# Performance work log

Measured on AMD Instinct MI355X. Metric: run time of the kernel, lower is better.

The kernel has to match this reference:

```python
import jax, jax.numpy as jnp
import numpy as np

N = 100_000      # nodes
E = 3_200_000    # edges
B = 1024         # graphs in batch
IN = 4           # in_channels
G = 16           # GCNNodes
D = 32           # NDenseNodes


def _linear_params(k, out_f, in_f):
    s = 1.0 / np.sqrt(in_f)
    kw, kb = jax.random.split(k)
    W = jax.random.uniform(kw, (out_f, in_f), jnp.float32, -s, s)
    b = jax.random.uniform(kb, (out_f,), jnp.float32, -s, s)
    return W, b


def setup_inputs() -> dict:
    key = jax.random.key(0)
    ks = jax.random.split(key, 12)
    X = jax.random.normal(ks[0], (N, IN), jnp.float32)
    Edge_index = jax.random.randint(ks[1], (2, E), 0, N, jnp.int64)
    Edge_weight = jax.random.uniform(ks[2], (E,), jnp.float32)
    Batching = jnp.sort(jax.random.randint(ks[3], (N,), 0, B, jnp.int64))
    W1, b1 = _linear_params(ks[4], G, IN)   # Conv1 lin (PyG GCNConv: Linear no bias + bias param)
    W2, b2 = _linear_params(ks[5], G, G)    # Conv2
    C1w, C1b = _linear_params(ks[6], D, 2 * G)
    C2w, C2b = _linear_params(ks[7], D, D)
    C3w, C3b = _linear_params(ks[8], 1, D)
    R1w, R1b = _linear_params(ks[9], D, 2 * G)
    R2w, R2b = _linear_params(ks[10], D, D)
    R3w, R3b = _linear_params(ks[11], 1, D)
    return {"X": X, "Edge_index": Edge_index, "Edge_weight": Edge_weight,
            "Batching": Batching, "num_graphs": B,
            "W1": W1, "b1": b1, "W2": W2, "b2": b2,
            "C1w": C1w, "C1b": C1b, "C2w": C2w, "C2b": C2b, "C3w": C3w, "C3b": C3b,
            "R1w": R1w, "R1b": R1b, "R2w": R2w, "R2b": R2b, "R3w": R3w, "R3b": R3b}


def _gcn_conv(x, row, col, w, W, b):
    """PyG GCNConv: add self loops (weight 1), symmetric norm, x@W.T, scatter-add at col, +b."""
    n = x.shape[0]
    loop = jnp.arange(n)
    row2 = jnp.concatenate([row, loop])
    col2 = jnp.concatenate([col, loop])
    w2 = jnp.concatenate([w, jnp.ones((n,), x.dtype)])
    deg = jax.ops.segment_sum(w2, col2, num_segments=n)          # deg >= 1 via self loops
    dinv = jnp.where(deg > 0, jax.lax.rsqrt(deg), 0.0)
    norm = dinv[row2] * w2 * dinv[col2]                           # [E+n]
    xw = x @ W.T                                                  # [n, out]
    out = jax.ops.segment_sum(norm[:, None] * xw[row2], col2, num_segments=n)
    return out + b


def reference(X, Edge_index, Edge_weight, Batching, num_graphs,
              W1, b1, W2, b2, C1w, C1b, C2w, C2b, C3w, C3b,
              R1w, R1b, R2w, R2b, R3w, R3b):
    act = jax.nn.leaky_relu  # default slope 0.01, matches nn.LeakyReLU()
    row, col = Edge_index[0], Edge_index[1]
    # add_self_loops then keep only col > row  ==  zero out weights where col <= row
    w = jnp.where(col > row, Edge_weight, 0.0)

    out = act(_gcn_conv(X, row, col, w, W1, b1))
    out = act(_gcn_conv(out, row, col, w, W2, b2))

    ones = jnp.ones((out.shape[0],), out.dtype)
    cnt = jax.ops.segment_sum(ones, Batching, num_segments=num_graphs)
    outMean = jax.ops.segment_sum(out, Batching, num_segments=num_graphs) / jnp.maximum(cnt, 1.0)[:, None]
    outMax = jax.ops.segment_max(out, Batching, num_segments=num_graphs)
    pooled = jnp.concatenate([outMean, outMax], axis=1)           # [B, 2G]

    Chi0 = act(pooled @ C1w.T + C1b)
    Chi0 = act(Chi0 @ C2w.T + C2b)
    Chi0 = Chi0 @ C3w.T + C3b
    Rp = act(pooled @ R1w.T + R1b)
    Rp = act(Rp @ R2w.T + R2b)
    Rp = Rp @ R3w.T + R3b
    return jnp.concatenate([Chi0, Rp], axis=1)                    # [B, 2]
```

## Files before the change

### kernel.cpp

```cpp
#include <hip/hip_runtime.h>
#include <hip/hip_bf16.h>
#include <float.h>

#define LRELU(x) ((x) > 0.0f ? (x) : 0.01f * (x))

typedef unsigned long long u64;

__global__ __launch_bounds__(256) void k_init(const float* __restrict__ X,
                                              const float* __restrict__ W1,
                                              u64* __restrict__ deg64,
                                              float* __restrict__ xw, int N) {
    int i = blockIdx.x * blockDim.x + threadIdx.x;
    if (i >= N) return;
    deg64[i] = (u64)1 << 32;
    const float4 x = *reinterpret_cast<const float4*>(X + 4 * i);
    float o[16];
#pragma unroll
    for (int g = 0; g < 16; ++g) {
        const float4 wr = *reinterpret_cast<const float4*>(W1 + 4 * g);
        o[g] = x.x * wr.x + x.y * wr.y + x.z * wr.z + x.w * wr.w;
    }
    float4* dst = reinterpret_cast<float4*>(xw + 16 * i);
#pragma unroll
    for (int k = 0; k < 4; ++k)
        dst[k] = make_float4(o[4 * k], o[4 * k + 1], o[4 * k + 2], o[4 * k + 3]);
}

__global__ __launch_bounds__(256) void k_count(const int* __restrict__ row,
                                               const int* __restrict__ col,
                                               const float* __restrict__ w,
                                               u64* __restrict__ deg64,
                                               unsigned char* __restrict__ rank, int E) {
    int e = blockIdx.x * blockDim.x + threadIdx.x;
    if (e >= E) return;
    int r = row[e], c = col[e];
    if (c <= r) return;
    u64 add = ((u64)1 << 40) | (u64)(w[e] * 4294967296.0f);
    u64 old = atomicAdd(deg64 + c, add);
    rank[e] = (unsigned char)(old >> 40);
}

__global__ __launch_bounds__(256) void k_scan1(const u64* __restrict__ deg64,
                                               int* __restrict__ offs,
                                               int* __restrict__ partials, int N) {
    __shared__ int sm[256];
    int tid = threadIdx.x;
    int base = blockIdx.x * 1024 + tid * 4;
    int v[4];
    int s = 0;
#pragma unroll
    for (int k = 0; k < 4; ++k) {
        int idx = base + k;
        v[k] = (idx < N) ? (int)(deg64[idx] >> 40) : 0;
        s += v[k];
    }
    sm[tid] = s;
    __syncthreads();
    for (int off = 1; off < 256; off <<= 1) {
        int t = (tid >= off) ? sm[tid - off] : 0;
        __syncthreads();
        sm[tid] += t;
        __syncthreads();
    }
    int run = sm[tid] - s;
#pragma unroll
    for (int k = 0; k < 4; ++k) {
        int idx = base + k;
        if (idx < N) offs[idx] = run;
        run += v[k];
    }
    if (tid == 255) partials[blockIdx.x] = sm[255];
}

__global__ __launch_bounds__(256) void k_scan2(int* __restrict__ partials,
                                               int* __restrict__ offs, int nb, int N) {
    __shared__ int sm[256];
    int tid = threadIdx.x;
    int v = (tid < nb) ? partials[tid] : 0;
    sm[tid] = v;
    __syncthreads();
    for (int off = 1; off < 256; off <<= 1) {
        int t = (tid >= off) ? sm[tid - off] : 0;
        __syncthreads();
        sm[tid] += t;
        __syncthreads();
    }
    if (tid < nb) partials[tid] = sm[tid] - v;
    if (tid == nb - 1) offs[N] = sm[tid];
}

__global__ __launch_bounds__(256) void k_self3(int* __restrict__ offs,
                                               const int* __restrict__ partials,
                                               const u64* __restrict__ deg64,
                                               float* __restrict__ dinv,
                                               const float* __restrict__ xw,
                                               float* __restrict__ acc, int N) {
    int i = blockIdx.x * blockDim.x + threadIdx.x;
    if (i >= N) return;
    offs[i] += partials[i >> 10];
    float wsum = (float)((double)(deg64[i] & (((u64)1 << 40) - 1)) * (1.0 / 4294967296.0));
    float d = rsqrtf(wsum);
    dinv[i] = d;
    float s = d * d;
    const float4* xs = reinterpret_cast<const float4*>(xw + 16 * i);
    float4* as = reinterpret_cast<float4*>(acc + 16 * i);
#pragma unroll
    for (int k = 0; k < 4; ++k) {
        float4 v = xs[k];
        as[k] = make_float4(s * v.x, s * v.y, s * v.z, s * v.w);
    }
}

__global__ __launch_bounds__(256) void k_fill(const int* __restrict__ row,
                                              const int* __restrict__ col,
                                              const float* __restrict__ w,
                                              const float* __restrict__ dinv,
                                              const int* __restrict__ offs,
                                              const unsigned char* __restrict__ rank,
                                              int2* __restrict__ pack, int E) {
    int e = blockIdx.x * blockDim.x + threadIdx.x;
    if (e >= E) return;
    int r = row[e], c = col[e];
    if (c <= r) return;
    float nrm = dinv[r] * w[e] * dinv[c];
    int pos = offs[c] + (int)rank[e];
    pack[pos] = make_int2(r, __float_as_int(nrm));
}

__global__ __launch_bounds__(256) void k_gather(const int* __restrict__ offs,
                                                const int2* __restrict__ pack,
                                                const float* __restrict__ xw,
                                                float* __restrict__ acc, int N) {
    int t = blockIdx.x * blockDim.x + threadIdx.x;
    if (t >= 16 * N) return;
    int c = t >> 4, g = t & 15;
    int beg = offs[c], end = offs[c + 1];
    float a = acc[t];
    for (int j = beg; j < end; ++j) {
        int2 p = pack[j];
        a += __int_as_float(p.y) * xw[((size_t)p.x << 4) + g];
    }
    acc[t] = a;
}

__global__ __launch_bounds__(256) void k_mid(const float* __restrict__ b1,
                                             const float* __restrict__ W2,
                                             const float* __restrict__ dinv,
                                             float* __restrict__ xw,
                                             float* __restrict__ acc, int N) {
    int i = blockIdx.x * blockDim.x + threadIdx.x;
    if (i >= N) return;
    float h[16];
#pragma unroll
    for (int g = 0; g < 16; ++g) {
        float v = acc[16 * i + g] + b1[g];
        h[g] = LRELU(v);
    }
    float d = dinv[i];
    float s = d * d;
#pragma unroll
    for (int g = 0; g < 16; ++g) {
        float a = 0.0f;
#pragma unroll
        for (int k = 0; k < 16; ++k) a += h[k] * W2[16 * g + k];
        xw[16 * i + g] = a;
        acc[16 * i + g] = s * a;
    }
}

__global__ __launch_bounds__(256) void k_initf(const float* __restrict__ X,
                                               const float* __restrict__ W1,
                                               float* __restrict__ deg,
                                               float* __restrict__ xw, int N) {
    int i = blockIdx.x * blockDim.x + threadIdx.x;
    if (i >= N) return;
    deg[i] = 1.0f;
    const float4 x = *reinterpret_cast<const float4*>(X + 4 * i);
    float o[16];
#pragma unroll
    for (int g = 0; g < 16; ++g) {
        const float4 wr = *reinterpret_cast<const float4*>(W1 + 4 * g);
        o[g] = x.x * wr.x + x.y * wr.y + x.z * wr.z + x.w * wr.w;
    }
    float4* dst = reinterpret_cast<float4*>(xw + 16 * i);
#pragma unroll
    for (int k = 0; k < 4; ++k)
        dst[k] = make_float4(o[4 * k], o[4 * k + 1], o[4 * k + 2], o[4 * k + 3]);
}

__global__ __launch_bounds__(256) void k_degf(const int* __restrict__ row,
                                              const int* __restrict__ col,
                                              const float* __restrict__ w,
                                              float* __restrict__ deg, int E) {
    int e = blockIdx.x * blockDim.x + threadIdx.x;
    if (e >= E) return;
    int r = row[e], c = col[e];
    if (c > r) atomicAdd(deg + c, w[e]);
}

__global__ __launch_bounds__(256) void k_self(float* __restrict__ deg_dinv,
                                              const float* __restrict__ xw,
                                              float* __restrict__ acc, int N) {
    int i = blockIdx.x * blockDim.x + threadIdx.x;
    if (i >= N) return;
    float d = rsqrtf(deg_dinv[i]);
    deg_dinv[i] = d;
    float s = d * d;
    const float4* xs = reinterpret_cast<const float4*>(xw + 16 * i);
    float4* as = reinterpret_cast<float4*>(acc + 16 * i);
#pragma unroll
    for (int k = 0; k < 4; ++k) {
        float4 v = xs[k];
        as[k] = make_float4(s * v.x, s * v.y, s * v.z, s * v.w);
    }
}

__global__ __launch_bounds__(256) void k_scatter(const int* __restrict__ row,
                                                 const int* __restrict__ col,
                                                 const float* __restrict__ w,
                                                 const float* __restrict__ dinv,
                                                 const float* __restrict__ xw,
                                                 float* __restrict__ acc, int E) {
    int e = blockIdx.x * blockDim.x + threadIdx.x;
    if (e >= E) return;
    int r = row[e], c = col[e];
    if (c <= r) return;
    float nrm = dinv[r] * w[e] * dinv[c];
    const float4* xr = reinterpret_cast<const float4*>(xw + 16 * r);
    float* ac = acc + 16 * c;
#pragma unroll
    for (int k = 0; k < 4; ++k) {
        float4 v = xr[k];
        atomicAdd(ac + 4 * k + 0, nrm * v.x);
        atomicAdd(ac + 4 * k + 1, nrm * v.y);
        atomicAdd(ac + 4 * k + 2, nrm * v.z);
        atomicAdd(ac + 4 * k + 3, nrm * v.w);
    }
}

__global__ __launch_bounds__(64) void k_pool(const float* __restrict__ acc,
                                             const float* __restrict__ b2,
                                             const int* __restrict__ batching,
                                             int N,
                                             const float* __restrict__ C1w, const float* __restrict__ C1b,
                                             const float* __restrict__ C2w, const float* __restrict__ C2b,
                                             const float* __restrict__ C3w, const float* __restrict__ C3b,
                                             const float* __restrict__ R1w, const float* __restrict__ R1b,
                                             const float* __restrict__ R2w, const float* __restrict__ R2b,
                                             const float* __restrict__ R3w, const float* __restrict__ R3b,
                                             float* __restrict__ out) {
    int b = blockIdx.x;
    int t = threadIdx.x;
    __shared__ int s_se[2];
    __shared__ float sp[32];
    __shared__ float h1s[64];
    __shared__ float h2s[64];
    if (t < 2) {
        int target = b + t;
        int lo = 0, hi = N;
        while (lo < hi) {
            int mid = (lo + hi) >> 1;
            if (batching[mid] < target) lo = mid + 1; else hi = mid;
        }
        s_se[t] = lo;
    }
    __syncthreads();
    int start = s_se[0], end = s_se[1];
    int g = t & 15, sub = t >> 4;
    float bg = b2[g];
    float sum = 0.0f, mx = -FLT_MAX;
    for (int n = start + sub; n < end; n += 4) {
        float v = acc[16 * n + g] + bg;
        v = LRELU(v);
        sum += v;
        mx = fmaxf(mx, v);
    }
    sum += __shfl_down(sum, 32);
    mx = fmaxf(mx, __shfl_down(mx, 32));
    sum += __shfl_down(sum, 16);
    mx = fmaxf(mx, __shfl_down(mx, 16));
    if (t < 16) {
        float cnt = (float)(end - start);
        sp[t] = sum / fmaxf(cnt, 1.0f);
        sp[16 + t] = mx;
    }
    __syncthreads();
    int d = t & 31;
    const float* W1h = (t < 32) ? C1w : R1w;
    const float* b1h = (t < 32) ? C1b : R1b;
    float a1 = b1h[d];
#pragma unroll 4
    for (int k = 0; k < 32; ++k) a1 += sp[k] * W1h[32 * d + k];
    h1s[t] = LRELU(a1);
    __syncthreads();
    const float* W2h = (t < 32) ? C2w : R2w;
    const float* b2h = (t < 32) ? C2b : R2b;
    const float* h1base = h1s + (t < 32 ? 0 : 32);
    float a2 = b2h[d];
#pragma unroll 4
    for (int k = 0; k < 32; ++k) a2 += h1base[k] * W2h[32 * d + k];
    h2s[t] = LRELU(a2);
    __syncthreads();
    if (t == 0 || t == 32) {
        const float* w3 = (t == 0) ? C3w : R3w;
        float a3 = (t == 0) ? C3b[0] : R3b[0];
        const float* hb = h2s + t;
#pragma unroll 4
        for (int k = 0; k < 32; ++k) a3 += hb[k] * w3[k];
        out[2 * b + (t >> 5)] = a3;
    }
}

extern "C" void kernel_launch(void* const* d_in, const int* in_sizes, int n_in,
                              void* d_out, int out_size, void* d_ws, size_t ws_size,
                              hipStream_t stream) {
    const float* X   = (const float*)d_in[0];
    const int*   EI  = (const int*)d_in[1];
    const float* EW  = (const float*)d_in[2];
    const int*   Bat = (const int*)d_in[3];
    const float* W1  = (const float*)d_in[5];
    const float* b1  = (const float*)d_in[6];
    const float* W2  = (const float*)d_in[7];
    const float* b2  = (const float*)d_in[8];
    const float* C1w = (const float*)d_in[9];
    const float* C1b = (const float*)d_in[10];
    const float* C2w = (const float*)d_in[11];
    const float* C2b = (const float*)d_in[12];
    const float* C3w = (const float*)d_in[13];
    const float* C3b = (const float*)d_in[14];
    const float* R1w = (const float*)d_in[15];
    const float* R1b = (const float*)d_in[16];
    const float* R2w = (const float*)d_in[17];
    const float* R2b = (const float*)d_in[18];
    const float* R3w = (const float*)d_in[19];
    const float* R3b = (const float*)d_in[20];

    const int N = in_sizes[0] / 4;
    const int E = in_sizes[1] / 2;
    const int B = out_size / 2;
    const int* row = EI;
    const int* col = EI + E;

    float* outp = (float*)d_out;

    size_t off = 0;
    u64*   deg64 = (u64*)d_ws;            off += 2 * (size_t)N;
    float* xw    = (float*)d_ws + off;    off += 16 * (size_t)N;
    float* acc   = (float*)d_ws + off;    off += 16 * (size_t)N;
    float* dinv  = (float*)d_ws + off;    off += (size_t)N;
    int*   offs  = (int*)d_ws + off;      off += (size_t)N + 1;
    int*   part  = (int*)d_ws + off;      off += 256;
    unsigned char* rank = (unsigned char*)((int*)d_ws + off);
    off += ((size_t)E + 3) / 4;
    off = (off + 1) & ~(size_t)1;
    int2*  pack  = (int2*)((int*)d_ws + off);
    size_t needed = off * 4 + (size_t)E * 8;

    const int nb = (N + 1023) / 1024;

    dim3 blk(256);
    dim3 gN((N + 255) / 256);
    dim3 gE((E + 255) / 256);
    dim3 gNG((16 * N + 255) / 256);

    if (needed <= ws_size && nb <= 256) {
        k_init <<<gN, blk, 0, stream>>>(X, W1, deg64, xw, N);
        k_count<<<gE, blk, 0, stream>>>(row, col, EW, deg64, rank, E);
        k_scan1<<<dim3(nb), blk, 0, stream>>>(deg64, offs, part, N);
        k_scan2<<<dim3(1), blk, 0, stream>>>(part, offs, nb, N);
        k_self3<<<gN, blk, 0, stream>>>(offs, part, deg64, dinv, xw, acc, N);
        k_fill <<<gE, blk, 0, stream>>>(row, col, EW, dinv, offs, rank, pack, E);
        k_gather<<<gNG, blk, 0, stream>>>(offs, pack, xw, acc, N);
        k_mid  <<<gN, blk, 0, stream>>>(b1, W2, dinv, xw, acc, N);
        k_gather<<<gNG, blk, 0, stream>>>(offs, pack, xw, acc, N);
        k_pool<<<dim3(B), dim3(64), 0, stream>>>(acc, b2, Bat, N,
                                                 C1w, C1b, C2w, C2b, C3w, C3b,
                                                 R1w, R1b, R2w, R2b, R3w, R3b,
                                                 outp);
    } else {
        float* deg = (float*)d_ws;
        k_initf<<<gN, blk, 0, stream>>>(X, W1, deg, xw, N);
        k_degf <<<gE, blk, 0, stream>>>(row, col, EW, deg, E);
        k_self <<<gN, blk, 0, stream>>>(deg, xw, acc, N);
        k_scatter<<<gE, blk, 0, stream>>>(row, col, EW, deg, xw, acc, E);
        k_mid  <<<gN, blk, 0, stream>>>(b1, W2, deg, xw, acc, N);
        k_scatter<<<gE, blk, 0, stream>>>(row, col, EW, deg, xw, acc, E);
        k_pool<<<dim3(B), dim3(64), 0, stream>>>(acc, b2, Bat, N,
                                                 C1w, C1b, C2w, C2b, C3w, C3b,
                                                 R1w, R1b, R2w, R2b, R3w, R3b,
                                                 outp);
    }
}
```

Baseline: 266.5 us.

## Fuse GCN pipeline kernels: merge init/count, fold dinv into scan, fuse gather with mid

Restructures the CSR-based GCN pipeline into fewer kernels. The xw1 projection now runs in extra blocks of the degree-count launch, and dinv is computed inside the first scan pass. Offset fixup runs alongside the edge fill. The self-loop term, bias, LeakyReLU and the W2 matmul (via wavefront shuffles) are fused into the first gather, and bias plus activation into the second. This removes several full-N passes over the 16-wide feature buffers and some launches, at the cost of more complex kernels and one extra offsets array.

```diff
diff --git a/kernel.cpp b/kernel.cpp
--- a/kernel.cpp
+++ b/kernel.cpp
@@ -5,54 +5,72 @@
 #define LRELU(x) ((x) > 0.0f ? (x) : 0.01f * (x))
 
 typedef unsigned long long u64;
-
-__global__ __launch_bounds__(256) void k_init(const float* __restrict__ X,
-                                              const float* __restrict__ W1,
-                                              u64* __restrict__ deg64,
-                                              float* __restrict__ xw, int N) {
+#define MASK40 (((u64)1 << 40) - 1)
+
+__global__ __launch_bounds__(256) void k_zero(u64* __restrict__ deg64, int N) {
     int i = blockIdx.x * blockDim.x + threadIdx.x;
-    if (i >= N) return;
-    deg64[i] = (u64)1 << 32;
-    const float4 x = *reinterpret_cast<const float4*>(X + 4 * i);
-    float o[16];
-#pragma unroll
-    for (int g = 0; g < 16; ++g) {
-        const float4 wr = *reinterpret_cast<const float4*>(W1 + 4 * g);
-        o[g] = x.x * wr.x + x.y * wr.y + x.z * wr.z + x.w * wr.w;
-    }
-    float4* dst = reinterpret_cast<float4*>(xw + 16 * i);
-#pragma unroll
-    for (int k = 0; k < 4; ++k)
-        dst[k] = make_float4(o[4 * k], o[4 * k + 1], o[4 * k + 2], o[4 * k + 3]);
-}
-
-__global__ __launch_bounds__(256) void k_count(const int* __restrict__ row,
-                                               const int* __restrict__ col,
-                                               const float* __restrict__ w,
-                                               u64* __restrict__ deg64,
-                                               unsigned char* __restrict__ rank, int E) {
-    int e = blockIdx.x * blockDim.x + threadIdx.x;
-    if (e >= E) return;
-    int r = row[e], c = col[e];
-    if (c <= r) return;
-    u64 add = ((u64)1 << 40) | (u64)(w[e] * 4294967296.0f);
-    u64 old = atomicAdd(deg64 + c, add);
-    rank[e] = (unsigned char)(old >> 40);
+    if (i < N) deg64[i] = (u64)1 << 32;
+}
+
+__global__ __launch_bounds__(256) void k_countx(const int* __restrict__ row,
+                                                const int* __restrict__ col,
+                                                const float* __restrict__ w,
+                                                const float* __restrict__ X,
+                                                const float* __restrict__ W1,
+                                                u64* __restrict__ deg64,
+                                                unsigned char* __restrict__ rank,
+                                                float* __restrict__ xw1,
+                                                int E, int N, int gE) {
+    int tid = threadIdx.x;
+    if ((int)blockIdx.x < gE) {
+        int e = blockIdx.x * 256 + tid;
+        if (e >= E) return;
+        int r = row[e], c = col[e];
+        if (c <= r) return;
+        u64 add = ((u64)1 << 40) | (u64)(w[e] * 4294967296.0f);
+        u64 old = atomicAdd(deg64 + c, add);
+        rank[e] = (unsigned char)(old >> 40);
+    } else {
+        int i = (blockIdx.x - gE) * 256 + tid;
+        if (i >= N) return;
+        const float4 x = *reinterpret_cast<const float4*>(X + 4 * i);
+        float o[16];
+#pragma unroll
+        for (int g = 0; g < 16; ++g) {
+            const float4 wr = *reinterpret_cast<const float4*>(W1 + 4 * g);
+            o[g] = x.x * wr.x + x.y * wr.y + x.z * wr.z + x.w * wr.w;
+        }
+        float4* dst = reinterpret_cast<float4*>(xw1 + 16 * i);
+#pragma unroll
+        for (int k = 0; k < 4; ++k)
+            dst[k] = make_float4(o[4 * k], o[4 * k + 1], o[4 * k + 2], o[4 * k + 3]);
+    }
 }
 
 __global__ __launch_bounds__(256) void k_scan1(const u64* __restrict__ deg64,
                                                int* __restrict__ offs,
-                                               int* __restrict__ partials, int N) {
+                                               int* __restrict__ partials,
+                                               float* __restrict__ dinv, int N) {
     __shared__ int sm[256];
     int tid = threadIdx.x;
     int base = blockIdx.x * 1024 + tid * 4;
     int v[4];
+    float dv[4];
     int s = 0;
 #pragma unroll
     for (int k = 0; k < 4; ++k) {
         int idx = base + k;
-        v[k] = (idx < N) ? (int)(deg64[idx] >> 40) : 0;
+        u64 d = (idx < N) ? deg64[idx] : ((u64)1 << 32);
+        v[k] = (int)(d >> 40);
+        float wsum = (float)((double)(d & MASK40) * (1.0 / 4294967296.0));
+        dv[k] = rsqrtf(wsum);
         s += v[k];
+    }
+    if (base + 3 < N) {
+        *reinterpret_cast<float4*>(dinv + base) = make_float4(dv[0], dv[1], dv[2], dv[3]);
+    } else {
+#pragma unroll
+        for (int k = 0; k < 4; ++k) if (base + k < N) dinv[base + k] = dv[k];
     }
     sm[tid] = s;
     __syncthreads();
@@ -89,166 +107,108 @@
     if (tid == nb - 1) offs[N] = sm[tid];
 }
 
-__global__ __launch_bounds__(256) void k_self3(int* __restrict__ offs,
-                                               const int* __restrict__ partials,
-                                               const u64* __restrict__ deg64,
-                                               float* __restrict__ dinv,
-                                               const float* __restrict__ xw,
-                                               float* __restrict__ acc, int N) {
-    int i = blockIdx.x * blockDim.x + threadIdx.x;
-    if (i >= N) return;
-    offs[i] += partials[i >> 10];
-    float wsum = (float)((double)(deg64[i] & (((u64)1 << 40) - 1)) * (1.0 / 4294967296.0));
-    float d = rsqrtf(wsum);
-    dinv[i] = d;
-    float s = d * d;
-    const float4* xs = reinterpret_cast<const float4*>(xw + 16 * i);
-    float4* as = reinterpret_cast<float4*>(acc + 16 * i);
-#pragma unroll
-    for (int k = 0; k < 4; ++k) {
-        float4 v = xs[k];
-        as[k] = make_float4(s * v.x, s * v.y, s * v.z, s * v.w);
-    }
-}
-
-__global__ __launch_bounds__(256) void k_fill(const int* __restrict__ row,
-                                              const int* __restrict__ col,
-                                              const float* __restrict__ w,
-                                              const float* __restrict__ dinv,
-                                              const int* __restrict__ offs,
-                                              const unsigned char* __restrict__ rank,
-                                              int2* __restrict__ pack, int E) {
-    int e = blockIdx.x * blockDim.x + threadIdx.x;
-    if (e >= E) return;
-    int r = row[e], c = col[e];
-    if (c <= r) return;
-    float nrm = dinv[r] * w[e] * dinv[c];
-    int pos = offs[c] + (int)rank[e];
-    pack[pos] = make_int2(r, __float_as_int(nrm));
-}
-
-__global__ __launch_bounds__(256) void k_gather(const int* __restrict__ offs,
-                                                const int2* __restrict__ pack,
-                                                const float* __restrict__ xw,
-                                                float* __restrict__ acc, int N) {
+__global__ __launch_bounds__(256) void k_fillx(const int* __restrict__ row,
+                                               const int* __restrict__ col,
+                                               const float* __restrict__ w,
+                                               const float* __restrict__ dinv,
+                                               const int* __restrict__ offs,
+                                               const int* __restrict__ part,
+                                               const unsigned char* __restrict__ rank,
+                                               int2* __restrict__ pack,
+                                               int* __restrict__ offsF,
+                                               int E, int N, int gE) {
+    int tid = threadIdx.x;
+    if ((int)blockIdx.x < gE) {
+        int e = blockIdx.x * 256 + tid;
+        if (e >= E) return;
+        int r = row[e], c = col[e];
+        if (c <= r) return;
+        float nrm = dinv[r] * w[e] * dinv[c];
+        int pos = offs[c] + part[c >> 10] + (int)rank[e];
+        pack[pos] = make_int2(r, __float_as_int(nrm));
+    } else {
+        int i = (blockIdx.x - gE) * 256 + tid;
+        if (i == 0) offsF[N] = offs[N];
+        if (i >= N) return;
+        offsF[i] = offs[i] + part[i >> 10];
+    }
+}
+
+__global__ __launch_bounds__(256) void k_gather1m(const int* __restrict__ offsF,
+                                                  const int2* __restrict__ pack,
+                                                  const float* __restrict__ xw1,
+                                                  const float* __restrict__ dinv,
+                                                  const float* __restrict__ b1,
+                                                  const float* __restrict__ W2,
+                                                  float* __restrict__ xw2, int N) {
+    int t = blockIdx.x * blockDim.x + threadIdx.x;
+    int NT = 16 * N;
+    bool valid = t < NT;
+    int tc = valid ? t : NT - 1;
+    int c = tc >> 4, g = tc & 15;
+    int beg = offsF[c], end = offsF[c + 1];
+    float d = dinv[c];
+    float a = d * d * xw1[tc];
+    for (int j = beg; j < end; ++j) {
+        int2 p = pack[j];
+        a += __int_as_float(p.y) * xw1[((size_t)p.x << 4) + g];
+    }
+    float h = a + b1[g];
+    h = LRELU(h);
+    int lane = threadIdx.x & 63;
+    int base = lane & 48;
+    const float4* W2r = reinterpret_cast<const float4*>(W2 + 16 * g);
+    float4 w0 = W2r[0], w1 = W2r[1], w2 = W2r[2], w3 = W2r[3];
+    float o = 0.0f;
+    o += __shfl(h, base + 0) * w0.x;
+    o += __shfl(h, base + 1) * w0.y;
+    o += __shfl(h, base + 2) * w0.z;
+    o += __shfl(h, base + 3) * w0.w;
+    o += __shfl(h, base + 4) * w1.x;
+    o += __shfl(h, base + 5) * w1.y;
+    o += __shfl(h, base + 6) * w1.z;
+    o += __shfl(h, base + 7) * w1.w;
+    o += __shfl(h, base + 8) * w2.x;
+    o += __shfl(h, base + 9) * w2.y;
+    o += __shfl(h, base + 10) * w2.z;
+    o += __shfl(h, base + 11) * w2.w;
+    o += __shfl(h, base + 12) * w3.x;
+    o += __shfl(h, base + 13) * w3.y;
+    o += __shfl(h, base + 14) * w3.z;
+    o += __shfl(h, base + 15) * w3.w;
+    if (valid) xw2[t] = o;
+}
+
+__global__ __launch_bounds__(256) void k_gather2(const int* __restrict__ offsF,
+                                                 const int2* __restrict__ pack,
+                                                 const float* __restrict__ xw2,
+                                                 const float* __restrict__ dinv,
+                                                 const float* __restrict__ b2,
+                                                 float* __restrict__ acc, int N) {
     int t = blockIdx.x * blockDim.x + threadIdx.x;
     if (t >= 16 * N) return;
     int c = t >> 4, g = t & 15;
-    int beg = offs[c], end = offs[c + 1];
-    float a = acc[t];
+    int beg = offsF[c], end = offsF[c + 1];
+    float d = dinv[c];
+    float a = d * d * xw2[t];
     for (int j = beg; j < end; ++j) {
         int2 p = pack[j];
-        a += __int_as_float(p.y) * xw[((size_t)p.x << 4) + g];
-    }
-    acc[t] = a;
-}
-
-__global__ __launch_bounds__(256) void k_mid(const float* __restrict__ b1,
-                                             const float* __restrict__ W2,
-                                             const float* __restrict__ dinv,
-                                             float* __restrict__ xw,
-                                             float* __restrict__ acc, int N) {
-    int i = blockIdx.x * blockDim.x + threadIdx.x;
-    if (i >= N) return;
-    float h[16];
-#pragma unroll
-    for (int g = 0; g < 16; ++g) {
-        float v = acc[16 * i + g] + b1[g];
-        h[g] = LRELU(v);
-    }
-    float d = dinv[i];
-    float s = d * d;
-#pragma unroll
-    for (int g = 0; g < 16; ++g) {
-        float a = 0.0f;
-#pragma unroll
-        for (int k = 0; k < 16; ++k) a += h[k] * W2[16 * g + k];
-        xw[16 * i + g] = a;
-        acc[16 * i + g] = s * a;
-    }
-}
-
-__global__ __launch_bounds__(256) void k_initf(const float* __restrict__ X,
-                                               const float* __restrict__ W1,
-                                               float* __restrict__ deg,
-                                               float* __restrict__ xw, int N) {
-    int i = blockIdx.x * blockDim.x + threadIdx.x;
-    if (i >= N) return;
-    deg[i] = 1.0f;
-    const float4 x = *reinterpret_cast<const float4*>(X + 4 * i);
-    float o[16];
-#pragma unroll
-    for (int g = 0; g < 16; ++g) {
-        const float4 wr = *reinterpret_cast<const float4*>(W1 + 4 * g);
-        o[g] = x.x * wr.x + x.y * wr.y + x.z * wr.z + x.w * wr.w;
-    }
-    float4* dst = reinterpret_cast<float4*>(xw + 16 * i);
-#pragma unroll
-    for (int k = 0; k < 4; ++k)
-        dst[k] = make_float4(o[4 * k], o[4 * k + 1], o[4 * k + 2], o[4 * k + 3]);
-}
-
-__global__ __launch_bounds__(256) void k_degf(const int* __restrict__ row,
-                                              const int* __restrict__ col,
-                                              const float* __restrict__ w,
-                                              float* __restrict__ deg, int E) {
-    int e = blockIdx.x * blockDim.x + threadIdx.x;
-    if (e >= E) return;
-    int r = row[e], c = col[e];
-    if (c > r) atomicAdd(deg + c, w[e]);
-}
-
-__global__ __launch_bounds__(256) void k_self(float* __restrict__ deg_dinv,
-                                              const float* __restrict__ xw,
-                                              float* __restrict__ acc, int N) {
-    int i = blockIdx.x * blockDim.x + threadIdx.x;
-    if (i >= N) return;
-    float d = rsqrtf(deg_dinv[i]);
-    deg_dinv[i] = d;
-    float s = d * d;
-    const float4* xs = reinterpret_cast<const float4*>(xw + 16 * i);
-    float4* as = reinterpret_cast<float4*>(acc + 16 * i);
-#pragma unroll
-    for (int k = 0; k < 4; ++k) {
-        float4 v = xs[k];
-        as[k] = make_float4(s * v.x, s * v.y, s * v.z, s * v.w);
-    }
-}
-
-__global__ __launch_bounds__(256) void k_scatter(const int* __restrict__ row,
-                                                 const int* __restrict__ col,
-                                                 const float* __restrict__ w,
-                                                 const float* __restrict__ dinv,
-                                                 const float* __restrict__ xw,
-                                                 float* __restrict__ acc, int E) {
-    int e = blockIdx.x * blockDim.x + threadIdx.x;
-    if (e >= E) return;
-    int r = row[e], c = col[e];
-    if (c <= r) return;
-    float nrm = dinv[r] * w[e] * dinv[c];
-    const float4* xr = reinterpret_cast<const float4*>(xw + 16 * r);
-    float* ac = acc + 16 * c;
-#pragma unroll
-    for (int k = 0; k < 4; ++k) {
-        float4 v = xr[k];
-        atomicAdd(ac + 4 * k + 0, nrm * v.x);
-        atomicAdd(ac + 4 * k + 1, nrm * v.y);
-        atomicAdd(ac + 4 * k + 2, nrm * v.z);
-        atomicAdd(ac + 4 * k + 3, nrm * v.w);
-    }
-}
-
-__global__ __launch_bounds__(64) void k_pool(const float* __restrict__ acc,
-                                             const float* __restrict__ b2,
-                                             const int* __restrict__ batching,
-                                             int N,
-                                             const float* __restrict__ C1w, const float* __restrict__ C1b,
-                                             const float* __restrict__ C2w, const float* __restrict__ C2b,
-                                             const float* __restrict__ C3w, const float* __restrict__ C3b,
-                                             const float* __restrict__ R1w, const float* __restrict__ R1b,
-                                             const float* __restrict__ R2w, const float* __restrict__ R2b,
-                                             const float* __restrict__ R3w, const float* __restrict__ R3b,
-                                             float* __restrict__ out) {
+        a += __int_as_float(p.y) * xw2[((size_t)p.x << 4) + g];
+    }
+    a += b2[g];
+    acc[t] = LRELU(a);
+}
+
+__global__ __launch_bounds__(64) void k_poolA(const float* __restrict__ acc,
+                                              const int* __restrict__ batching,
+                                              int N,
+                                              const float* __restrict__ C1w, const float* __restrict__ C1b,
+                                              const float* __restrict__ C2w, const float* __restrict__ C2b,
+                                              const float* __restrict__ C3w, const float* __restrict__ C3b,
+                                              const float* __restrict__ R1w, const float* __restrict__ R1b,
+                                              const float* __restrict__ R2w, const float* __restrict__ R2b,
+                                              const float* __restrict__ R3w, const float* __restrict__ R3b,
+                                              float* __restrict__ out) {
     int b = blockIdx.x;
     int t = threadIdx.x;
     __shared__ int s_se[2];
@@ -267,11 +227,9 @@
     __syncthreads();
     int start = s_se[0], end = s_se[1];
     int g = t & 15, sub = t >> 4;
-    float bg = b2[g];
     float sum = 0.0f, mx = -FLT_MAX;
     for (int n = start + sub; n < end; n += 4) {
-        float v = acc[16 * n + g] + bg;
-        v = LRELU(v);
+        float v = acc[16 * n + g];
         sum += v;
         mx = fmaxf(mx, v);
     }
@@ -309,6 +267,109 @@
         for (int k = 0; k < 32; ++k) a3 += hb[k] * w3[k];
         out[2 * b + (t >> 5)] = a3;
     }
+}
+
+__global__ __launch_bounds__(256) void k_initf(const float* __restrict__ X,
+                                               const float* __restrict__ W1,
+                                               float* __restrict__ deg,
+                                               float* __restrict__ xw, int N) {
+    int i = blockIdx.x * blockDim.x + threadIdx.x;
+    if (i >= N) return;
+    deg[i] = 1.0f;
+    const float4 x = *reinterpret_cast<const float4*>(X + 4 * i);
+    float o[16];
+#pragma unroll
+    for (int g = 0; g < 16; ++g) {
+        const float4 wr = *reinterpret_cast<const float4*>(W1 + 4 * g);
+        o[g] = x.x * wr.x + x.y * wr.y + x.z * wr.z + x.w * wr.w;
+    }
+    float4* dst = reinterpret_cast<float4*>(xw + 16 * i);
+#pragma unroll
+    for (int k = 0; k < 4; ++k)
+        dst[k] = make_float4(o[4 * k], o[4 * k + 1], o[4 * k + 2], o[4 * k + 3]);
+}
+
+__global__ __launch_bounds__(256) void k_degf(const int* __restrict__ row,
+                                              const int* __restrict__ col,
+                                              const float* __restrict__ w,
+                                              float* __restrict__ deg, int E) {
+    int e = blockIdx.x * blockDim.x + threadIdx.x;
+    if (e >= E) return;
+    int r = row[e], c = col[e];
+    if (c > r) atomicAdd(deg + c, w[e]);
+}
+
+__global__ __launch_bounds__(256) void k_self(float* __restrict__ deg_dinv,
+                                              const float* __restrict__ xw,
+                                              float* __restrict__ acc, int N) {
+    int i = blockIdx.x * blockDim.x + threadIdx.x;
+    if (i >= N) return;
+    float d = rsqrtf(deg_dinv[i]);
+    deg_dinv[i] = d;
+    float s = d * d;
+    const float4* xs = reinterpret_cast<const float4*>(xw + 16 * i);
+    float4* as = reinterpret_cast<float4*>(acc + 16 * i);
+#pragma unroll
+    for (int k = 0; k < 4; ++k) {
+        float4 v = xs[k];
+        as[k] = make_float4(s * v.x, s * v.y, s * v.z, s * v.w);
+    }
+}
+
+__global__ __launch_bounds__(256) void k_scatter(const int* __restrict__ row,
+                                                 const int* __restrict__ col,
+                                                 const float* __restrict__ w,
+                                                 const float* __restrict__ dinv,
+                                                 const float* __restrict__ xw,
+                                                 float* __restrict__ acc, int E) {
+    int e = blockIdx.x * blockDim.x + threadIdx.x;
+    if (e >= E) return;
+    int r = row[e], c = col[e];
+    if (c <= r) return;
+    float nrm = dinv[r] * w[e] * dinv[c];
+    const float4* xr = reinterpret_cast<const float4*>(xw + 16 * r);
+    float* ac = acc + 16 * c;
+#pragma unroll
+    for (int k = 0; k < 4; ++k) {
+        float4 v = xr[k];
+        atomicAdd(ac + 4 * k + 0, nrm * v.x);
+        atomicAdd(ac + 4 * k + 1, nrm * v.y);
+        atomicAdd(ac + 4 * k + 2, nrm * v.z);
+        atomicAdd(ac + 4 * k + 3, nrm * v.w);
+    }
+}
+
+__global__ __launch_bounds__(256) void k_mid(const float* __restrict__ b1,
+                                             const float* __restrict__ W2,
+                                             const float* __restrict__ dinv,
+                                             float* __restrict__ xw,
+                                             float* __restrict__ acc, int N) {
+    int i = blockIdx.x * blockDim.x + threadIdx.x;
+    if (i >= N) return;
+    float h[16];
+#pragma unroll
+    for (int g = 0; g < 16; ++g) {
+        float v = acc[16 * i + g] + b1[g];
+        h[g] = LRELU(v);
+    }
+    float d = dinv[i];
+    float s = d * d;
+#pragma unroll
+    for (int g = 0; g < 16; ++g) {
+        float a = 0.0f;
+#pragma unroll
+        for (int k = 0; k < 16; ++k) a += h[k] * W2[16 * g + k];
+        xw[16 * i + g] = a;
+        acc[16 * i + g] = s * a;
+    }
+}
+
+__global__ __launch_bounds__(256) void k_act(const float* __restrict__ b2,
+                                             float* __restrict__ acc, int NT) {
+    int t = blockIdx.x * blockDim.x + threadIdx.x;
+    if (t >= NT) return;
+    float v = acc[t] + b2[t & 15];
+    acc[t] = LRELU(v);
 }
 
 extern "C" void kernel_launch(void* const* d_in, const int* in_sizes, int n_in,
@@ -345,10 +406,11 @@
 
     size_t off = 0;
     u64*   deg64 = (u64*)d_ws;            off += 2 * (size_t)N;
-    float* xw    = (float*)d_ws + off;    off += 16 * (size_t)N;
-    float* acc   = (float*)d_ws + off;    off += 16 * (size_t)N;
+    float* xw1   = (float*)d_ws + off;    off += 16 * (size_t)N;
+    float* xw2   = (float*)d_ws + off;    off += 16 * (size_t)N;
     float* dinv  = (float*)d_ws + off;    off += (size_t)N;
     int*   offs  = (int*)d_ws + off;      off += (size_t)N + 1;
+    int*   offsF = (int*)d_ws + off;      off += (size_t)N + 1;
     int*   part  = (int*)d_ws + off;      off += 256;
     unsigned char* rank = (unsigned char*)((int*)d_ws + off);
     off += ((size_t)E + 3) / 4;
@@ -359,35 +421,39 @@
     const int nb = (N + 1023) / 1024;
 
     dim3 blk(256);
-    dim3 gN((N + 255) / 256);
-    dim3 gE((E + 255) / 256);
-    dim3 gNG((16 * N + 255) / 256);
+    const int gN  = (N + 255) / 256;
+    const int gE  = (E + 255) / 256;
+    const int gNG = (16 * N + 255) / 256;
 
     if (needed <= ws_size && nb <= 256) {
-        k_init <<<gN, blk, 0, stream>>>(X, W1, deg64, xw, N);
-        k_count<<<gE, blk, 0, stream>>>(row, col, EW, deg64, rank, E);
-        k_scan1<<<dim3(nb), blk, 0, stream>>>(deg64, offs, part, N);
-        k_scan2<<<dim3(1), blk, 0, stream>>>(part, offs, nb, N);
-        k_self3<<<gN, blk, 0, stream>>>(offs, part, deg64, dinv, xw, acc, N);
-        k_fill <<<gE, blk, 0, stream>>>(row, col, EW, dinv, offs, rank, pack, E);
-        k_gather<<<gNG, blk, 0, stream>>>(offs, pack, xw, acc, N);
-        k_mid  <<<gN, blk, 0, stream>>>(b1, W2, dinv, xw, acc, N);
-        k_gather<<<gNG, blk, 0, stream>>>(offs, pack, xw, acc, N);
-        k_pool<<<dim3(B), dim3(64), 0, stream>>>(acc, b2, Bat, N,
-                                                 C1w, C1b, C2w, C2b, C3w, C3b,
-                                                 R1w, R1b, R2w, R2b, R3w, R3b,
-                                                 outp);
+        float* acc = xw1;
+        k_zero  <<<dim3(gN), blk, 0, stream>>>(deg64, N);
+        k_countx<<<dim3(gE + gN), blk, 0, stream>>>(row, col, EW, X, W1,
+                                                    deg64, rank, xw1, E, N, gE);
+        k_scan1 <<<dim3(nb), blk, 0, stream>>>(deg64, offs, part, dinv, N);
+        k_scan2 <<<dim3(1), blk, 0, stream>>>(part, offs, nb, N);
+        k_fillx <<<dim3(gE + gN), blk, 0, stream>>>(row, col, EW, dinv, offs, part,
+                                                    rank, pack, offsF, E, N, gE);
+        k_gather1m<<<dim3(gNG), blk, 0, stream>>>(offsF, pack, xw1, dinv, b1, W2, xw2, N);
+        k_gather2 <<<dim3(gNG), blk, 0, stream>>>(offsF, pack, xw2, dinv, b2, acc, N);
+        k_poolA <<<dim3(B), dim3(64), 0, stream>>>(acc, Bat, N,
+                                                   C1w, C1b, C2w, C2b, C3w, C3b,
+                                                   R1w, R1b, R2w, R2b, R3w, R3b,
+                                                   outp);
     } else {
         float* deg = (float*)d_ws;
-        k_initf<<<gN, blk, 0, stream>>>(X, W1, deg, xw, N);
-        k_degf <<<gE, blk, 0, stream>>>(row, col, EW, deg, E);
-        k_self <<<gN, blk, 0, stream>>>(deg, xw, acc, N);
-        k_scatter<<<gE, blk, 0, stream>>>(row, col, EW, deg, xw, acc, E);
-        k_mid  <<<gN, blk, 0, stream>>>(b1, W2, deg, xw, acc, N);
-        k_scatter<<<gE, blk, 0, stream>>>(row, col, EW, deg, xw, acc, E);
-        k_pool<<<dim3(B), dim3(64), 0, stream>>>(acc, b2, Bat, N,
-                                                 C1w, C1b, C2w, C2b, C3w, C3b,
-                                                 R1w, R1b, R2w, R2b, R3w, R3b,
-                                                 outp);
-    }
-}
+        float* xw  = (float*)d_ws + N;
+        float* acc = xw + 16 * (size_t)N;
+        k_initf<<<dim3(gN), blk, 0, stream>>>(X, W1, deg, xw, N);
+        k_degf <<<dim3(gE), blk, 0, stream>>>(row, col, EW, deg, E);
+        k_self <<<dim3(gN), blk, 0, stream>>>(deg, xw, acc, N);
+        k_scatter<<<dim3(gE), blk, 0, stream>>>(row, col, EW, deg, xw, acc, E);
+        k_mid  <<<dim3(gN), blk, 0, stream>>>(b1, W2, deg, xw, acc, N);
+        k_scatter<<<dim3(gE), blk, 0, stream>>>(row, col, EW, deg, xw, acc, E);
+        k_act  <<<dim3(gNG), blk, 0, stream>>>(b2, acc, 16 * N);
+        k_poolA<<<dim3(B), dim3(64), 0, stream>>>(acc, Bat, N,
+                                                  C1w, C1b, C2w, C2b, C3w, C3b,
+                                                  R1w, R1b, R2w, R2b, R3w, R3b,
+                                                  outp);
+    }
+}
```

Result: faster. 252.5 us (-5.3%).
